# Kernel tuning notes

Measured on AMD Instinct MI355X. Metric: run time of the kernel, lower is better.

## Reference

```python
import jax, jax.numpy as jnp
import numpy as np

C, H, W = 9, 180, 240          # dim = (C, H, W)
IMAGE_SIZE = 640
N_EVENTS = 250_000
B = 8
NEG_SLOPE = 0.1


def setup_inputs() -> dict:
    key = jax.random.key(0)
    kx, ky, kt, kp, kb, k1, k2, k3, k4, k5, k6 = jax.random.split(key, 11)
    x = jax.random.randint(kx, (N_EVENTS,), 0, W).astype(jnp.float32)
    y = jax.random.randint(ky, (N_EVENTS,), 0, H).astype(jnp.float32)
    t = jax.random.uniform(kt, (N_EVENTS,), minval=1e-3, maxval=1.0)
    p = jax.random.randint(kp, (N_EVENTS,), 0, 2).astype(jnp.float32)
    b = jax.random.randint(kb, (N_EVENTS,), 0, B)
    b = b.at[-1].set(B - 1)  # forward derives B from the last event's batch id
    events = jnp.stack([x, y, t, p, b.astype(jnp.float32)], axis=1)
    # value-layer MLP params (Linear stored as [in, out] so h @ W + b)
    W1 = jax.random.normal(k1, (1, 100), jnp.float32)      # fan_in = 1
    b1 = jax.random.normal(k2, (100,), jnp.float32) * 0.1
    W2 = jax.random.normal(k3, (100, 100), jnp.float32) * 0.1
    b2 = jax.random.normal(k4, (100,), jnp.float32) * 0.1
    W3 = jax.random.normal(k5, (100, 1), jnp.float32) * 0.1
    b3 = jax.random.normal(k6, (1,), jnp.float32) * 0.1
    return {"events": events, "W1": W1, "b1": b1, "W2": W2, "b2": b2,
            "W3": W3, "b3": b3, "batch_size": B}


def _value_layer(ts, W1, b1, W2, b2, W3, b3):
    # ValueLayer.forward: x[None,...,None] -> two LeakyReLU(0.1) layers -> final linear -> squeeze
    h = ts[..., None]                                   # [N, 1]
    h = jax.nn.leaky_relu(h @ W1 + b1, NEG_SLOPE)       # [N, 100]
    h = jax.nn.leaky_relu(h @ W2 + b2, NEG_SLOPE)       # [N, 100]
    return (h @ W3 + b3)[..., 0]                        # [N]


def reference(events, W1, b1, W2, b2, W3, b3, batch_size):
    x, y, t, p, b = (events[:, i] for i in range(5))
    bid = b.astype(jnp.int32)
    # per-batch max-normalization of timestamps
    bmax = jax.ops.segment_max(t, bid, num_segments=batch_size)
    t = t / bmax[bid]
    num_voxels = 2 * C * H * W * batch_size
    idx_before_bins = x + W * y + W * H * C * p + W * H * C * 2 * b
    vox = jnp.zeros((num_voxels,), jnp.float32)
    for i_bin in range(C):  # fixed small structural loop over temporal bins
        values = t * _value_layer(t - i_bin / (C - 1), W1, b1, W2, b2, W3, b3)
        idx = jnp.clip((idx_before_bins + W * H * i_bin).astype(jnp.int32), 0, num_voxels - 1)
        vox = vox.at[idx].add(values)  # atomic scatter-add (put_ accumulate)
    vox = vox.reshape(batch_size, 2, C, H, W)
    vox = jnp.concatenate([vox[:, 0], vox[:, 1]], axis=1)  # [B, 2C, H, W]
    # letterbox to IMAGE_SIZE x IMAGE_SIZE (bilinear, align_corners=False == half-pixel)
    scale = min(IMAGE_SIZE / W, IMAGE_SIZE / H)
    new_w, new_h = int(W * scale), int(H * scale)
    resized = jax.image.resize(vox, (batch_size, 2 * C, new_h, new_w), method="bilinear")
    top, left = (IMAGE_SIZE - new_h) // 2, (IMAGE_SIZE - new_w) // 2
    out = jnp.full((batch_size, 2 * C, IMAGE_SIZE, IMAGE_SIZE), 114.0, jnp.float32)
    out = out.at[:, :, top:top + new_h, left:left + new_w].set(resized)
    return out
```

## Files before the change

### kernel.cpp

```cpp
#include <hip/hip_runtime.h>

#define C_BINS 9
#define H_IN 180
#define W_IN 240
#define IMG 640
#define NEV 250000
#define BATCH 8
#define NEG_SLOPE 0.1f
#define HW (H_IN * W_IN)
#define TN 2048
#define ROWF (W_IN * C_BINS)
#define NROW (2 * BATCH * H_IN)
#define CAP 512
#define OVF_CAP 4096

#define WS_BMAX_OFF   0
#define WS_OVFC_OFF   64
#define WS_TABLE_OFF  128
#define WS_CUR_OFF    16384
#define WS_BKT_OFF    262144
#define WS_OVF_OFF    12582912

__global__ __launch_bounds__(128) void prep_kernel(
        const float* __restrict__ W1, const float* __restrict__ b1,
        const float* __restrict__ W2, const float* __restrict__ b2,
        const float* __restrict__ W3, const float* __restrict__ b3,
        float* __restrict__ table, int* __restrict__ cursor,
        int* __restrict__ ovfc) {
    int blk = blockIdx.x, tid = threadIdx.x;
    int gtid = blk * 128 + tid;
    int gstride = gridDim.x * 128;
    for (int i = gtid; i < NROW * 16; i += gstride) cursor[i] = 0;
    if (gtid == 0) *ovfc = 0;

    __shared__ float h1s[100];
    __shared__ float red[128];
    float s = -1.f + 2.f * (float)blk / (float)TN;
    if (tid < 100) {
        float h = fmaf(s, W1[tid], b1[tid]);
        h1s[tid] = h > 0.f ? h : NEG_SLOPE * h;
    }
    __syncthreads();
    float acc = 0.f;
    if (tid < 100) {
        #pragma unroll 4
        for (int j = 0; j < 100; ++j) acc = fmaf(h1s[j], W2[j * 100 + tid], acc);
        acc += b2[tid];
        acc = acc > 0.f ? acc : NEG_SLOPE * acc;
        acc *= W3[tid];
    }
    red[tid] = tid < 100 ? acc : 0.f;
    __syncthreads();
    for (int off = 64; off > 0; off >>= 1) {
        if (tid < off) red[tid] += red[tid + off];
        __syncthreads();
    }
    if (tid == 0) table[blk] = red[0] + b3[0];
}

__global__ __launch_bounds__(256) void place_kernel(const float* __restrict__ ev,
                               int* __restrict__ cursor,
                               float2* __restrict__ bucket,
                               int* __restrict__ bmax_i,
                               int* __restrict__ ovfc,
                               float4* __restrict__ ovf) {
    int i = blockIdx.x * 256 + threadIdx.x;
    int tid = threadIdx.x;
    __shared__ int smax[BATCH];
    if (tid < BATCH) smax[tid] = 0;
    __syncthreads();
    if (i < NEV) {
        float x = ev[i * 5 + 0];
        float y = ev[i * 5 + 1];
        float t = ev[i * 5 + 2];
        float p = ev[i * 5 + 3];
        int   b = (int)ev[i * 5 + 4];
        atomicMax(&smax[b & (BATCH - 1)], __float_as_int(t));
        int xi = min(max((int)x, 0), W_IN - 1);
        int row = (b * 2 + (int)p) * H_IN + (int)y;
        row = min(max(row, 0), NROW - 1);
        int pos = atomicAdd(&cursor[row * 16], 1);
        if (pos < CAP) {
            bucket[(size_t)row * CAP + pos] = make_float2(t, (float)xi);
        } else {
            int opos = atomicAdd(ovfc, 1);
            if (opos < OVF_CAP)
                ovf[opos] = make_float4(t, (float)xi, (float)row, 0.f);
        }
    }
    __syncthreads();
    if (tid < BATCH) atomicMax(&bmax_i[tid], smax[tid]);
}

__global__ __launch_bounds__(256) void fused_kernel(const float2* __restrict__ bucket,
                               const int* __restrict__ cursor,
                               const int* __restrict__ bmax_i,
                               const float* __restrict__ table,
                               const float4* __restrict__ ovf,
                               const int* __restrict__ ovfc,
                               float* __restrict__ out) {
    __shared__ float sm[5 * ROWF];
    int blk = blockIdx.x;
    int tid = threadIdx.x;

    if (blk >= 960) {
        const float4 v114 = make_float4(114.f, 114.f, 114.f, 114.f);
        float4* out4 = (float4*)out;
        int j0 = (blk - 960) * 12800 + tid;
        for (int j = j0; j < (blk - 960 + 1) * 12800; j += 256) {
            int plane = j / 25600;
            int rem = j - plane * 25600;
            int row = rem / 160;
            int col = rem - row * 160;
            if (row >= 80) row += 480;
            out4[((size_t)plane * IMG + row) * 160 + col] = v114;
        }
        return;
    }

    int b   = blk / 120;
    int rem = blk - b * 120;
    int p   = rem / 60;
    int yt  = rem - p * 60;
    int ry0 = yt * 8;
    float sy0 = fmaf((float)ry0 + 0.5f, 0.375f, -0.5f);
    int ybase = (int)floorf(sy0);
    int rowbase = (b * 2 + p) * H_IN;
    float bm = __int_as_float(bmax_i[b]);

    for (int c = tid; c < 5 * ROWF; c += 256) sm[c] = 0.f;
    __syncthreads();

    #pragma unroll
    for (int r = 0; r < 5; ++r) {
        int sr = min(max(ybase + r, 0), H_IN - 1);
        int row = rowbase + sr;
        int count = min(cursor[row * 16], CAP);
        for (int e = tid; e < count; e += 256) {
            float2 pay = bucket[(size_t)row * CAP + e];
            float tn = pay.x / bm;
            int xi = (int)pay.y;
            float u0 = (tn + 1.f) * (0.5f * (float)TN);
            int k0 = (int)floorf(u0);
            float f = u0 - (float)k0;
            #pragma unroll
            for (int bin = 0; bin < C_BINS; ++bin) {
                int k = k0 - 128 * bin;
                float fb = f;
                if (k >= TN) { k = TN - 1; fb = 1.f; }
                if (k < 0)   { k = 0;      fb = 0.f; }
                float t0 = table[k], t1 = table[k + 1];
                float g = fmaf(t1 - t0, fb, t0);
                atomicAdd(&sm[r * ROWF + xi * C_BINS + bin], tn * g);
            }
        }
    }
    int n = min(*ovfc, OVF_CAP);
    for (int j = tid; j < n; j += 256) {
        float4 pay = ovf[j];
        int orow = (int)pay.z;
        #pragma unroll
        for (int r = 0; r < 5; ++r) {
            int sr = min(max(ybase + r, 0), H_IN - 1);
            if (orow != rowbase + sr) continue;
            float tn = pay.x / bm;
            int xi = (int)pay.y;
            float u0 = (tn + 1.f) * (0.5f * (float)TN);
            int k0 = (int)floorf(u0);
            float f = u0 - (float)k0;
            for (int bin = 0; bin < C_BINS; ++bin) {
                int k = k0 - 128 * bin;
                float fb = f;
                if (k >= TN) { k = TN - 1; fb = 1.f; }
                if (k < 0)   { k = 0;      fb = 0.f; }
                float t0 = table[k], t1 = table[k + 1];
                float g = fmaf(t1 - t0, fb, t0);
                atomicAdd(&sm[r * ROWF + xi * C_BINS + bin], tn * g);
            }
        }
    }
    __syncthreads();

    int PB = b * 18 + p * 9;
    for (int g = tid; g < 1280; g += 256) {
        int row = g / 160;
        int gx = g - row * 160;
        int ry = ry0 + row;
        float sy = fmaf((float)ry + 0.5f, 0.375f, -0.5f);
        int y0 = (int)floorf(sy);
        float wy = sy - (float)y0;
        const float* r0 = sm + (max(y0, 0) - ybase) * ROWF;
        const float* r1 = sm + (min(y0 + 1, H_IN - 1) - ybase) * ROWF;
        float res[C_BINS][4];
        #pragma unroll
        for (int q = 0; q < 4; ++q) {
            int ox = gx * 4 + q;
            float sx = fmaf((float)ox + 0.5f, 0.375f, -0.5f);
            int x0 = (int)floorf(sx);
            float wx = sx - (float)x0;
            int x1 = min(x0 + 1, W_IN - 1);
            x0 = max(x0, 0);
            int o0 = x0 * C_BINS, o1 = x1 * C_BINS;
            #pragma unroll
            for (int bin = 0; bin < C_BINS; ++bin) {
                float v00 = r0[o0 + bin], v01 = r0[o1 + bin];
                float v10 = r1[o0 + bin], v11 = r1[o1 + bin];
                float top = fmaf(v01 - v00, wx, v00);
                float bot = fmaf(v11 - v10, wx, v10);
                res[bin][q] = fmaf(bot - top, wy, top);
            }
        }
        int oy = 80 + ry;
        #pragma unroll
        for (int bin = 0; bin < C_BINS; ++bin) {
            float4* dst = (float4*)(out + ((size_t)(PB + bin) * IMG + oy) * IMG);
            dst[gx] = make_float4(res[bin][0], res[bin][1], res[bin][2], res[bin][3]);
        }
    }
}

extern "C" void kernel_launch(void* const* d_in, const int* in_sizes, int n_in,
                              void* d_out, int out_size, void* d_ws, size_t ws_size,
                              hipStream_t stream) {
    const float* ev = (const float*)d_in[0];
    const float* W1 = (const float*)d_in[1];
    const float* b1 = (const float*)d_in[2];
    const float* W2 = (const float*)d_in[3];
    const float* b2 = (const float*)d_in[4];
    const float* W3 = (const float*)d_in[5];
    const float* b3 = (const float*)d_in[6];
    float* out = (float*)d_out;

    char* ws = (char*)d_ws;
    int*    bmax_i = (int*)(ws + WS_BMAX_OFF);
    int*    ovfc   = (int*)(ws + WS_OVFC_OFF);
    float*  table  = (float*)(ws + WS_TABLE_OFF);
    int*    cursor = (int*)(ws + WS_CUR_OFF);
    float2* bucket = (float2*)(ws + WS_BKT_OFF);
    float4* ovf    = (float4*)(ws + WS_OVF_OFF);

    prep_kernel<<<TN + 1, 128, 0, stream>>>(W1, b1, W2, b2, W3, b3,
                                            table, cursor, ovfc);
    place_kernel<<<(NEV + 255) / 256, 256, 0, stream>>>(ev, cursor, bucket,
                                                        bmax_i, ovfc, ovf);
    fused_kernel<<<960 + 288, 256, 0, stream>>>(bucket, cursor, bmax_i, table,
                                                ovf, ovfc, out);
}
```

Baseline: 300.8 us.

## Fuse MLP table build into place kernel, cache table in LDS, simplify resize

Moves the value-layer MLP table computation out of the prep kernel and into the place kernel, where blocks compute table nodes after placing their events. This shrinks the prep kernel to a vectorized zero fill. The fused kernel now copies the table into shared memory and multiplies by a reciprocal of bmax instead of dividing. The resize stage emits 8 outputs per thread from 5 source columns using the constant bilinear weights of the 3/8 scale, cutting LDS reads. The MLP loop adds extra syncthreads and serial work to every place block. The reciprocal multiply can differ slightly from the reference division.

```diff
diff --git a/kernel.cpp b/kernel.cpp
--- a/kernel.cpp
+++ b/kernel.cpp
@@ -13,6 +13,7 @@
 #define NROW (2 * BATCH * H_IN)
 #define CAP 512
 #define OVF_CAP 4096
+#define PLACE_NB ((NEV + 255) / 256)
 
 #define WS_BMAX_OFF   0
 #define WS_OVFC_OFF   64
@@ -21,52 +22,30 @@
 #define WS_BKT_OFF    262144
 #define WS_OVF_OFF    12582912
 
-__global__ __launch_bounds__(128) void prep_kernel(
-        const float* __restrict__ W1, const float* __restrict__ b1,
-        const float* __restrict__ W2, const float* __restrict__ b2,
-        const float* __restrict__ W3, const float* __restrict__ b3,
-        float* __restrict__ table, int* __restrict__ cursor,
-        int* __restrict__ ovfc) {
-    int blk = blockIdx.x, tid = threadIdx.x;
-    int gtid = blk * 128 + tid;
-    int gstride = gridDim.x * 128;
-    for (int i = gtid; i < NROW * 16; i += gstride) cursor[i] = 0;
+__global__ __launch_bounds__(256) void prep_zero(int4* __restrict__ cur4,
+                                                 int* __restrict__ ovfc) {
+    int gtid = blockIdx.x * 256 + threadIdx.x;
+    int gstride = gridDim.x * 256;
+    int4 z = make_int4(0, 0, 0, 0);
+    for (int i = gtid; i < NROW * 4; i += gstride) cur4[i] = z;
     if (gtid == 0) *ovfc = 0;
-
-    __shared__ float h1s[100];
-    __shared__ float red[128];
-    float s = -1.f + 2.f * (float)blk / (float)TN;
-    if (tid < 100) {
-        float h = fmaf(s, W1[tid], b1[tid]);
-        h1s[tid] = h > 0.f ? h : NEG_SLOPE * h;
-    }
-    __syncthreads();
-    float acc = 0.f;
-    if (tid < 100) {
-        #pragma unroll 4
-        for (int j = 0; j < 100; ++j) acc = fmaf(h1s[j], W2[j * 100 + tid], acc);
-        acc += b2[tid];
-        acc = acc > 0.f ? acc : NEG_SLOPE * acc;
-        acc *= W3[tid];
-    }
-    red[tid] = tid < 100 ? acc : 0.f;
-    __syncthreads();
-    for (int off = 64; off > 0; off >>= 1) {
-        if (tid < off) red[tid] += red[tid + off];
-        __syncthreads();
-    }
-    if (tid == 0) table[blk] = red[0] + b3[0];
 }
 
 __global__ __launch_bounds__(256) void place_kernel(const float* __restrict__ ev,
+                               const float* __restrict__ W1, const float* __restrict__ b1,
+                               const float* __restrict__ W2, const float* __restrict__ b2,
+                               const float* __restrict__ W3, const float* __restrict__ b3,
                                int* __restrict__ cursor,
                                float2* __restrict__ bucket,
                                int* __restrict__ bmax_i,
                                int* __restrict__ ovfc,
-                               float4* __restrict__ ovf) {
+                               float4* __restrict__ ovf,
+                               float* __restrict__ table) {
     int i = blockIdx.x * 256 + threadIdx.x;
     int tid = threadIdx.x;
     __shared__ int smax[BATCH];
+    __shared__ float h1s[100];
+    __shared__ float red[256];
     if (tid < BATCH) smax[tid] = 0;
     __syncthreads();
     if (i < NEV) {
@@ -90,6 +69,30 @@
     }
     __syncthreads();
     if (tid < BATCH) atomicMax(&bmax_i[tid], smax[tid]);
+
+    for (int node = blockIdx.x; node <= TN; node += PLACE_NB) {
+        float s = -1.f + 2.f * (float)node / (float)TN;
+        if (tid < 100) {
+            float h = fmaf(s, W1[tid], b1[tid]);
+            h1s[tid] = h > 0.f ? h : NEG_SLOPE * h;
+        }
+        __syncthreads();
+        float acc = 0.f;
+        if (tid < 100) {
+            #pragma unroll 4
+            for (int j = 0; j < 100; ++j) acc = fmaf(h1s[j], W2[j * 100 + tid], acc);
+            acc += b2[tid];
+            acc = acc > 0.f ? acc : NEG_SLOPE * acc;
+            acc *= W3[tid];
+        }
+        red[tid] = tid < 100 ? acc : 0.f;
+        __syncthreads();
+        for (int off = 128; off > 0; off >>= 1) {
+            if (tid < off) red[tid] += red[tid + off];
+            __syncthreads();
+        }
+        if (tid == 0) table[node] = red[0] + b3[0];
+    }
 }
 
 __global__ __launch_bounds__(256) void fused_kernel(const float2* __restrict__ bucket,
@@ -100,6 +103,7 @@
                                const int* __restrict__ ovfc,
                                float* __restrict__ out) {
     __shared__ float sm[5 * ROWF];
+    __shared__ float smt[TN + 1];
     int blk = blockIdx.x;
     int tid = threadIdx.x;
 
@@ -126,9 +130,10 @@
     float sy0 = fmaf((float)ry0 + 0.5f, 0.375f, -0.5f);
     int ybase = (int)floorf(sy0);
     int rowbase = (b * 2 + p) * H_IN;
-    float bm = __int_as_float(bmax_i[b]);
+    float rbm = 1.0f / __int_as_float(bmax_i[b]);
 
     for (int c = tid; c < 5 * ROWF; c += 256) sm[c] = 0.f;
+    for (int c = tid; c <= TN; c += 256) smt[c] = table[c];
     __syncthreads();
 
     #pragma unroll
@@ -138,9 +143,9 @@
         int count = min(cursor[row * 16], CAP);
         for (int e = tid; e < count; e += 256) {
             float2 pay = bucket[(size_t)row * CAP + e];
-            float tn = pay.x / bm;
+            float tn = pay.x * rbm;
             int xi = (int)pay.y;
-            float u0 = (tn + 1.f) * (0.5f * (float)TN);
+            float u0 = fmaf(tn, 1024.f, 1024.f);
             int k0 = (int)floorf(u0);
             float f = u0 - (float)k0;
             #pragma unroll
@@ -149,7 +154,7 @@
                 float fb = f;
                 if (k >= TN) { k = TN - 1; fb = 1.f; }
                 if (k < 0)   { k = 0;      fb = 0.f; }
-                float t0 = table[k], t1 = table[k + 1];
+                float t0 = smt[k], t1 = smt[k + 1];
                 float g = fmaf(t1 - t0, fb, t0);
                 atomicAdd(&sm[r * ROWF + xi * C_BINS + bin], tn * g);
             }
@@ -163,9 +168,9 @@
         for (int r = 0; r < 5; ++r) {
             int sr = min(max(ybase + r, 0), H_IN - 1);
             if (orow != rowbase + sr) continue;
-            float tn = pay.x / bm;
+            float tn = pay.x * rbm;
             int xi = (int)pay.y;
-            float u0 = (tn + 1.f) * (0.5f * (float)TN);
+            float u0 = fmaf(tn, 1024.f, 1024.f);
             int k0 = (int)floorf(u0);
             float f = u0 - (float)k0;
             for (int bin = 0; bin < C_BINS; ++bin) {
@@ -173,7 +178,7 @@
                 float fb = f;
                 if (k >= TN) { k = TN - 1; fb = 1.f; }
                 if (k < 0)   { k = 0;      fb = 0.f; }
-                float t0 = table[k], t1 = table[k + 1];
+                float t0 = smt[k], t1 = smt[k + 1];
                 float g = fmaf(t1 - t0, fb, t0);
                 atomicAdd(&sm[r * ROWF + xi * C_BINS + bin], tn * g);
             }
@@ -182,39 +187,44 @@
     __syncthreads();
 
     int PB = b * 18 + p * 9;
-    for (int g = tid; g < 1280; g += 256) {
-        int row = g / 160;
-        int gx = g - row * 160;
+    for (int item = tid; item < 640; item += 256) {
+        int row = item / 80;
+        int grp = item - row * 80;
         int ry = ry0 + row;
         float sy = fmaf((float)ry + 0.5f, 0.375f, -0.5f);
         int y0 = (int)floorf(sy);
         float wy = sy - (float)y0;
         const float* r0 = sm + (max(y0, 0) - ybase) * ROWF;
         const float* r1 = sm + (min(y0 + 1, H_IN - 1) - ybase) * ROWF;
-        float res[C_BINS][4];
-        #pragma unroll
-        for (int q = 0; q < 4; ++q) {
-            int ox = gx * 4 + q;
-            float sx = fmaf((float)ox + 0.5f, 0.375f, -0.5f);
-            int x0 = (int)floorf(sx);
-            float wx = sx - (float)x0;
-            int x1 = min(x0 + 1, W_IN - 1);
-            x0 = max(x0, 0);
-            int o0 = x0 * C_BINS, o1 = x1 * C_BINS;
-            #pragma unroll
-            for (int bin = 0; bin < C_BINS; ++bin) {
-                float v00 = r0[o0 + bin], v01 = r0[o1 + bin];
-                float v10 = r1[o0 + bin], v11 = r1[o1 + bin];
-                float top = fmaf(v01 - v00, wx, v00);
-                float bot = fmaf(v11 - v10, wx, v10);
-                res[bin][q] = fmaf(bot - top, wy, top);
-            }
-        }
+        int k3 = grp * 3;
+        int cs0 = max(k3 - 1, 0) * C_BINS;
+        int cs1 = k3 * C_BINS;
+        int cs2 = cs1 + C_BINS;
+        int cs3 = cs2 + C_BINS;
+        int cs4 = min(k3 + 3, W_IN - 1) * C_BINS;
         int oy = 80 + ry;
         #pragma unroll
         for (int bin = 0; bin < C_BINS; ++bin) {
-            float4* dst = (float4*)(out + ((size_t)(PB + bin) * IMG + oy) * IMG);
-            dst[gx] = make_float4(res[bin][0], res[bin][1], res[bin][2], res[bin][3]);
+            float a0 = r0[cs0 + bin], a1 = r0[cs1 + bin], a2 = r0[cs2 + bin],
+                  a3 = r0[cs3 + bin], a4 = r0[cs4 + bin];
+            float b0 = r1[cs0 + bin], b1v = r1[cs1 + bin], b2v = r1[cs2 + bin],
+                  b3v = r1[cs3 + bin], b4 = r1[cs4 + bin];
+            float v0 = fmaf(b0 - a0, wy, a0);
+            float v1 = fmaf(b1v - a1, wy, a1);
+            float v2 = fmaf(b2v - a2, wy, a2);
+            float v3 = fmaf(b3v - a3, wy, a3);
+            float v4 = fmaf(b4 - a4, wy, a4);
+            float o0 = fmaf(v1 - v0, 0.6875f, v0);
+            float o1 = fmaf(v2 - v1, 0.0625f, v1);
+            float o2 = fmaf(v2 - v1, 0.4375f, v1);
+            float o3 = fmaf(v2 - v1, 0.8125f, v1);
+            float o4 = fmaf(v3 - v2, 0.1875f, v2);
+            float o5 = fmaf(v3 - v2, 0.5625f, v2);
+            float o6 = fmaf(v3 - v2, 0.9375f, v2);
+            float o7 = fmaf(v4 - v3, 0.3125f, v3);
+            float4* d = (float4*)(out + ((size_t)(PB + bin) * IMG + oy) * IMG) + grp * 2;
+            d[0] = make_float4(o0, o1, o2, o3);
+            d[1] = make_float4(o4, o5, o6, o7);
         }
     }
 }
@@ -239,10 +249,10 @@
     float2* bucket = (float2*)(ws + WS_BKT_OFF);
     float4* ovf    = (float4*)(ws + WS_OVF_OFF);
 
-    prep_kernel<<<TN + 1, 128, 0, stream>>>(W1, b1, W2, b2, W3, b3,
-                                            table, cursor, ovfc);
-    place_kernel<<<(NEV + 255) / 256, 256, 0, stream>>>(ev, cursor, bucket,
-                                                        bmax_i, ovfc, ovf);
+    prep_zero<<<46, 256, 0, stream>>>((int4*)cursor, ovfc);
+    place_kernel<<<PLACE_NB, 256, 0, stream>>>(ev, W1, b1, W2, b2, W3, b3,
+                                               cursor, bucket, bmax_i, ovfc, ovf,
+                                               table);
     fused_kernel<<<960 + 288, 256, 0, stream>>>(bucket, cursor, bmax_i, table,
                                                 ovf, ovfc, out);
 }
```

Measured after the change: 324.0 us. 7.7% more time.
